# Performance work log

Measured on AMD Instinct MI355X. Metric: run time of the kernel, lower is better.

The kernel has to match this reference:

```python
import jax, jax.numpy as jnp
import numpy as np

B, T, C, H = 128, 200, 171, 1024  # batch, timesteps, frame_dim, hidden


def setup_inputs() -> dict:
    key = jax.random.key(0)
    ks = jax.random.split(key, 16)
    s = 1.0 / np.sqrt(H)  # PyTorch default init range for LSTMCell/Linear

    def u(k, shape):
        return jax.random.uniform(k, shape, jnp.float32, -s, s)

    inp = {
        "seq": jax.random.normal(ks[0], (B, T, C), jnp.float32),
        # LSTMCell 1: input C -> hidden H
        "W_ih1": u(ks[1], (4 * H, C)), "W_hh1": u(ks[2], (4 * H, H)),
        "b_ih1": u(ks[3], (4 * H,)),   "b_hh1": u(ks[4], (4 * H,)),
        # LSTMCell 2: H -> H
        "W_ih2": u(ks[5], (4 * H, H)), "W_hh2": u(ks[6], (4 * H, H)),
        "b_ih2": u(ks[7], (4 * H,)),   "b_hh2": u(ks[8], (4 * H,)),
        # LSTMCell 3: H -> H
        "W_ih3": u(ks[9], (4 * H, H)), "W_hh3": u(ks[10], (4 * H, H)),
        "b_ih3": u(ks[11], (4 * H,)),  "b_hh3": u(ks[12], (4 * H,)),
        # decoder Linear: H -> C
        "W_dec": u(ks[13], (C, H)), "b_dec": u(ks[14], (C,)),
        "cond": 5, "gt": 5,
    }
    return inp


def _lstm_cell(x, h, c, W_ih, W_hh, b_ih, b_hh):
    # PyTorch LSTMCell gate order: i, f, g, o
    gates = x @ W_ih.T + b_ih + h @ W_hh.T + b_hh
    i, f, g, o = jnp.split(gates, 4, axis=-1)
    c_new = jax.nn.sigmoid(f) * c + jax.nn.sigmoid(i) * jnp.tanh(g)
    h_new = jax.nn.sigmoid(o) * jnp.tanh(c_new)
    return h_new, c_new


def reference(seq, W_ih1, W_hh1, b_ih1, b_hh1,
              W_ih2, W_hh2, b_ih2, b_hh2,
              W_ih3, W_hh3, b_ih3, b_hh3,
              W_dec, b_dec, cond, gt):
    Bb, Tt, Cc = seq.shape
    Hh = W_hh1.shape[1]
    # Static teacher-forcing pattern: gt ground-truth steps, then cond self-conditioned steps.
    pattern = jnp.asarray(np.array(([True] * gt + [False] * cond) * 100, dtype=bool)[:Tt])

    def step(carry, xs):
        h1, c1, h2, c2, h3, c3, xo = carry
        x_t, use_gt = xs
        x = jnp.where(use_gt, x_t, xo)
        h1, c1 = _lstm_cell(x, h1, c1, W_ih1, W_hh1, b_ih1, b_hh1)
        h2, c2 = _lstm_cell(h1, h2, c2, W_ih2, W_hh2, b_ih2, b_hh2)
        h3, c3 = _lstm_cell(h2, h3, c3, W_ih3, W_hh3, b_ih3, b_hh3)
        xo = h3 @ W_dec.T + b_dec
        return (h1, c1, h2, c2, h3, c3, xo), xo

    z = jnp.zeros((Bb, Hh), seq.dtype)
    init = (z, z, z, z, z, z, jnp.zeros((Bb, Cc), seq.dtype))
    _, out = jax.lax.scan(step, init, (seq.transpose(1, 0, 2), pattern))
    return out.transpose(1, 0, 2)  # [B, T, C]
```

## Files before the change

### kernel.cpp

```cpp
#include <hip/hip_runtime.h>

#define TT 200
#define BB 128
#define CC 171
#define HH 1024

typedef __attribute__((ext_vector_type(8))) short short8;
typedef __attribute__((ext_vector_type(4))) float f32x4;

__device__ __forceinline__ unsigned short f2bf(float f) {
  unsigned int u = __float_as_uint(f);
  u += 0x7fff + ((u >> 16) & 1);
  return (unsigned short)(u >> 16);
}
__device__ __forceinline__ float sigmoidf_(float x) { return 1.f / (1.f + __expf(-x)); }

__device__ __forceinline__ int4 ld_coh16(const void* p) {
  int4 r;
  asm volatile("global_load_dwordx4 %0, %1, off sc0 sc1" : "=v"(r) : "v"(p));
  return r;
}
__device__ __forceinline__ void st_coh2(void* p, unsigned int v) {
  asm volatile("global_store_short %0, %1, off sc0 sc1" :: "v"(p), "v"(v) : "memory");
}
__device__ __forceinline__ void drain_vm() {
  asm volatile("s_waitcnt vmcnt(0)" ::: "memory");
}

__device__ __forceinline__ void gridbar(int* bar, int wg, int tid, int epoch) {
  drain_vm();
  __syncthreads();
  if (tid == 0) {
    int g = wg & 7;
    int o = __hip_atomic_fetch_add(&bar[g * 32], 1, __ATOMIC_RELAXED, __HIP_MEMORY_SCOPE_AGENT);
    if (o == epoch * 32 - 1) {
      int m = __hip_atomic_fetch_add(&bar[960], 1, __ATOMIC_RELAXED, __HIP_MEMORY_SCOPE_AGENT);
      if (m == epoch * 8 - 1) {
#pragma unroll
        for (int i = 0; i < 8; ++i)
          __hip_atomic_store(&bar[(16 + i) * 32], epoch, __ATOMIC_RELAXED, __HIP_MEMORY_SCOPE_AGENT);
      }
    }
    while (__hip_atomic_load(&bar[(16 + g) * 32], __ATOMIC_RELAXED, __HIP_MEMORY_SCOPE_AGENT) < epoch)
      __builtin_amdgcn_s_sleep(1);
  }
  asm volatile("" ::: "memory");
  __syncthreads();
}

template<int NKT1, int NKTTOT, bool A1SEQ>
__device__ __forceinline__ void lstm_phase(
    const void* A1v, int sA1,
    const unsigned short* __restrict__ A2, int sA2,
    const unsigned short* __restrict__ Wa, int sWa,
    const unsigned short* __restrict__ Wb, int sWb,
    const float* __restrict__ bias,
    float& creg, unsigned short* __restrict__ Hout,
    char* smem, int m0, int n0, int ntile, int tid)
{
  constexpr int BASE = NKTTOT / 4;
  constexpr int REM = NKTTOT % 4;
  constexpr int MAXKT = BASE + (REM ? 1 : 0);

  const int wave = tid >> 6, lane = tid & 63;
  const int grp = wave >> 2, gw = wave & 3;
  const int lrow = lane >> 3, lj = lane & 7;
  const int fl = lane & 15, fh = lane >> 4;

  const int kt0 = grp * BASE + min(grp, REM);
  const int ktn = BASE + (grp < REM ? 1 : 0);

  char* Ar = smem + grp * 32768;
  const int row = gw * 8 + lrow;
  int4 areg[MAXKT];
#pragma unroll
  for (int i = 0; i < MAXKT; ++i) {
    if (i < ktn) {
      int kt = kt0 + i;
      if (kt < NKT1) {
        if constexpr (A1SEQ) {
          const float* srow = (const float*)A1v + (size_t)(m0 + row) * sA1;
          int c0 = kt * 64 + ((lj ^ (row & 7)) << 3);
          unsigned int w[4];
#pragma unroll
          for (int j = 0; j < 4; ++j) {
            int ca = c0 + 2 * j, cb = c0 + 2 * j + 1;
            float va = (ca < CC) ? srow[ca] : 0.f;
            float vb = (cb < CC) ? srow[cb] : 0.f;
            w[j] = (unsigned int)f2bf(va) | ((unsigned int)f2bf(vb) << 16);
          }
          areg[i] = make_int4(w[0], w[1], w[2], w[3]);
        } else {
          const unsigned short* srow = (const unsigned short*)A1v + (size_t)(m0 + row) * sA1;
          areg[i] = ld_coh16(srow + kt * 64 + ((lj ^ (row & 7)) << 3));
        }
      } else {
        areg[i] = ld_coh16(A2 + (size_t)(m0 + row) * sA2 + (kt - NKT1) * 64 + ((lj ^ (row & 7)) << 3));
      }
    }
  }
  drain_vm();
#pragma unroll
  for (int i = 0; i < MAXKT; ++i)
    if (i < ktn) *(int4*)(Ar + i * 4096 + row * 128 + lj * 16) = areg[i];
  __syncthreads();

  f32x4 acc0 = {0.f, 0.f, 0.f, 0.f}, acc1 = {0.f, 0.f, 0.f, 0.f};
  const int wrowi = n0 + gw * 16 + fl;
  const int swz = (fl & 7) << 4;
#pragma unroll
  for (int i = 0; i < MAXKT; ++i) {
    if (i < ktn) {
      int kt = kt0 + i;
      const unsigned short* wr = (kt < NKT1)
          ? Wa + (size_t)wrowi * sWa + kt * 64 + fh * 8
          : Wb + (size_t)wrowi * sWb + (kt - NKT1) * 64 + fh * 8;
#pragma unroll
      for (int kk = 0; kk < 2; ++kk) {
        short8 b0 = *(const short8*)(wr + kk * 32);
        int colb = kk * 64 + fh * 16;
        short8 a0 = *(const short8*)(Ar + i * 4096 + fl * 128 + (colb ^ swz));
        short8 a1 = *(const short8*)(Ar + i * 4096 + (16 + fl) * 128 + (colb ^ swz));
        acc0 = __builtin_amdgcn_mfma_f32_16x16x32_bf16(a0, b0, acc0, 0, 0, 0);
        acc1 = __builtin_amdgcn_mfma_f32_16x16x32_bf16(a1, b0, acc1, 0, 0, 0);
      }
    }
  }

  __syncthreads();
  float* ex = (float*)smem;
#pragma unroll
  for (int r = 0; r < 4; ++r) {
    ex[((grp * 4 + gw) * 32 + fh * 4 + r) * 16 + fl] = acc0[r];
    ex[((grp * 4 + gw) * 32 + 16 + fh * 4 + r) * 16 + fl] = acc1[r];
  }
  __syncthreads();
  if (tid < 512) {
    int urow = tid >> 4, uu = tid & 15;
    float g4[4];
#pragma unroll
    for (int gg = 0; gg < 4; ++gg) {
      float s = ex[(gg * 32 + urow) * 16 + uu] + ex[((4 + gg) * 32 + urow) * 16 + uu]
              + ex[((8 + gg) * 32 + urow) * 16 + uu] + ex[((12 + gg) * 32 + urow) * 16 + uu];
      g4[gg] = s + bias[n0 + gg * 16 + uu];
    }
    float cn = sigmoidf_(g4[1]) * creg + sigmoidf_(g4[0]) * tanhf(g4[2]);
    creg = cn;
    st_coh2(Hout + (size_t)(m0 + urow) * HH + ntile * 16 + uu,
            (unsigned int)f2bf(sigmoidf_(g4[3]) * tanhf(cn)));
  }
}

__device__ __forceinline__ void dec_out(
    const unsigned short* __restrict__ H3in, const unsigned short* __restrict__ Wd,
    const float* __restrict__ bd, float* __restrict__ out,
    int t, char* smem, int d, int tid)
{
  const int wave = tid >> 6, lane = tid & 63;
  const int lrow = lane >> 3, lj = lane & 7;
  const int fl = lane & 15, fh = lane >> 4;
  const int ntile = d % 11, mtile = d / 11;
  const int m0 = mtile * 32, n0 = ntile * 16;

  char* Dr = smem + 65536 + wave * 4096;
  int4 r4[4];
#pragma unroll
  for (int j = 0; j < 4; ++j) {
    int row = j * 8 + lrow;
    r4[j] = ld_coh16(H3in + (size_t)(m0 + row) * HH + wave * 64 + ((lj ^ (row & 7)) << 3));
  }
  drain_vm();
#pragma unroll
  for (int j = 0; j < 4; ++j) {
    int row = j * 8 + lrow;
    *(int4*)(Dr + row * 128 + lj * 16) = r4[j];
  }

  f32x4 acc0 = {0.f, 0.f, 0.f, 0.f}, acc1 = {0.f, 0.f, 0.f, 0.f};
  const unsigned short* Wrow = Wd + (size_t)(n0 + fl) * HH + wave * 64 + fh * 8;
  const int swz = (fl & 7) << 4;
#pragma unroll
  for (int kk = 0; kk < 2; ++kk) {
    short8 b0 = *(const short8*)(Wrow + kk * 32);
    int colb = kk * 64 + fh * 16;
    short8 a0 = *(const short8*)(Dr + fl * 128 + (colb ^ swz));
    short8 a1 = *(const short8*)(Dr + (16 + fl) * 128 + (colb ^ swz));
    acc0 = __builtin_amdgcn_mfma_f32_16x16x32_bf16(a0, b0, acc0, 0, 0, 0);
    acc1 = __builtin_amdgcn_mfma_f32_16x16x32_bf16(a1, b0, acc1, 0, 0, 0);
  }

  float* pex = (float*)(smem + 32768);
#pragma unroll
  for (int r = 0; r < 4; ++r) {
    pex[(wave * 32 + fh * 4 + r) * 16 + fl] = acc0[r];
    pex[(wave * 32 + 16 + fh * 4 + r) * 16 + fl] = acc1[r];
  }
  __syncthreads();
  if (tid < 512) {
    int row = tid >> 4, uu = tid & 15;
    int c = n0 + uu;
    if (c < CC) {
      float s = 0.f;
#pragma unroll
      for (int v = 0; v < 16; ++v) s += pex[(v * 32 + row) * 16 + uu];
      out[(size_t)(m0 + row) * (TT * CC) + (size_t)t * CC + c] = s + bd[c];
    }
  }
}

__global__ __launch_bounds__(1024, 1) void persistent_lstm(
    const unsigned short* __restrict__ Wih1p, const unsigned short* __restrict__ Whh1,
    const unsigned short* __restrict__ Wf, const unsigned short* __restrict__ W2,
    const unsigned short* __restrict__ W3, const unsigned short* __restrict__ Wd,
    const float* __restrict__ B1gt, const float* __restrict__ B1sc,
    const float* __restrict__ B2, const float* __restrict__ B3, const float* __restrict__ Bd,
    unsigned short* __restrict__ Hb, const float* __restrict__ seq, float* __restrict__ out,
    const int* __restrict__ gtp, const int* __restrict__ condp, int* __restrict__ bar)
{
  __shared__ char smem[131072];
  const int wg = blockIdx.x, tid = threadIdx.x;
  const int xg = wg & 7, sl = wg >> 3;
  const int ntile = xg * 8 + (sl >> 2);
  const int m0 = (sl & 3) * 32;
  const int n0 = ntile * 64;
  const int gt = *gtp, cond = *condp;
  const int per = gt + cond;

  int decid = -1;
  if (sl >= 26) { int d = xg * 6 + (sl - 26); if (d < 44) decid = d; }

  unsigned short* H1[2] = { Hb + 0 * BB * HH, Hb + 1 * BB * HH };
  unsigned short* H2[2] = { Hb + 2 * BB * HH, Hb + 3 * BB * HH };
  unsigned short* H3[2] = { Hb + 4 * BB * HH, Hb + 5 * BB * HH };

  float c1 = 0.f, c2 = 0.f, c3 = 0.f;
  int e = 0, tm = 0;
  for (int t = 0; t < TT; ++t) {
    int p = t & 1;
    bool gts = (per > 0) ? (tm < gt) : true;
    if (gts)
      lstm_phase<3, 19, true>(seq + (size_t)t * CC, TT * CC, H1[p], HH,
                              Wih1p, 192, Whh1, HH, B1gt, c1, H1[1 - p], smem, m0, n0, ntile, tid);
    else
      lstm_phase<16, 32, false>(H3[p], HH, H1[p], HH,
                                Wf, HH, Whh1, HH, B1sc, c1, H1[1 - p], smem, m0, n0, ntile, tid);
    if (t > 0 && decid >= 0) dec_out(H3[p], Wd, Bd, out, t - 1, smem, decid, tid);
    gridbar(bar, wg, tid, ++e);
    lstm_phase<16, 32, false>(H1[1 - p], HH, H2[p], HH,
                              W2, 2048, W2 + 1024, 2048, B2, c2, H2[1 - p], smem, m0, n0, ntile, tid);
    gridbar(bar, wg, tid, ++e);
    lstm_phase<16, 32, false>(H2[1 - p], HH, H3[p], HH,
                              W3, 2048, W3 + 1024, 2048, B3, c3, H3[1 - p], smem, m0, n0, ntile, tid);
    gridbar(bar, wg, tid, ++e);
    if (++tm == per) tm = 0;
  }
  if (decid >= 0) dec_out(H3[0], Wd, Bd, out, TT - 1, smem, decid, tid);
}

__device__ __forceinline__ int perm_orig_row(int np) {
  return ((np >> 4) & 3) * HH + ((np >> 6) << 4) + (np & 15);
}

__global__ void conv_wih1p(const float* __restrict__ Wih, unsigned short* __restrict__ dst) {
  int np = blockIdx.x, k = threadIdx.x;
  int n = perm_orig_row(np);
  dst[(size_t)np * 192 + k] = f2bf((k < CC) ? Wih[(size_t)n * CC + k] : 0.f);
}

__global__ void conv_whh1(const float* __restrict__ Whh, unsigned short* __restrict__ dst) {
  int np = blockIdx.y, k = blockIdx.x * 256 + threadIdx.x;
  int n = perm_orig_row(np);
  dst[(size_t)np * HH + k] = f2bf(Whh[(size_t)n * HH + k]);
}

__global__ void conv_w23(const float* __restrict__ Wih, const float* __restrict__ Whh,
                         unsigned short* __restrict__ dst) {
  int k = blockIdx.x * 256 + threadIdx.x;
  int np = blockIdx.y;
  int n = perm_orig_row(np);
  float v = (k < HH) ? Wih[(size_t)n * HH + k] : Whh[(size_t)n * HH + (k - HH)];
  dst[(size_t)np * 2048 + k] = f2bf(v);
}

__global__ void conv_wd(const float* __restrict__ Wsrc, unsigned short* __restrict__ dst) {
  int k = blockIdx.x * 256 + threadIdx.x;
  int row = blockIdx.y;
  dst[(size_t)row * HH + k] = f2bf((row < CC) ? Wsrc[(size_t)row * HH + k] : 0.f);
}

__global__ void wf_gemm(const float* __restrict__ Wih1, const float* __restrict__ Wdec,
                        unsigned short* __restrict__ Wfo) {
  int j = blockIdx.x * 256 + threadIdx.x;
  int np = blockIdx.y;
  int n = perm_orig_row(np);
  const float* wr = Wih1 + (size_t)n * CC;
  float acc = 0.f;
  for (int c = 0; c < CC; ++c) acc = fmaf(wr[c], Wdec[(size_t)c * HH + j], acc);
  Wfo[(size_t)np * HH + j] = f2bf(acc);
}

__global__ void bias_all(const float* bi1, const float* bh1, const float* Wih1, const float* bdec,
                         const float* bi2, const float* bh2, const float* bi3, const float* bh3,
                         float* o1gt, float* o1sc, float* o2, float* o3, float* od) {
  int idx = blockIdx.x * 256 + threadIdx.x;
  if (idx < 4096) {
    int n = perm_orig_row(idx);
    float b = bi1[n] + bh1[n];
    o1gt[idx] = b;
    const float* wr = Wih1 + (size_t)n * CC;
    float acc = 0.f;
    for (int c = 0; c < CC; ++c) acc = fmaf(wr[c], bdec[c], acc);
    o1sc[idx] = b + acc;
  } else if (idx < 8192) {
    int np = idx - 4096; int n = perm_orig_row(np);
    o2[np] = bi2[n] + bh2[n];
  } else if (idx < 12288) {
    int np = idx - 8192; int n = perm_orig_row(np);
    o3[np] = bi3[n] + bh3[n];
  } else if (idx < 12464) {
    int c2 = idx - 12288;
    od[c2] = (c2 < CC) ? bdec[c2] : 0.f;
  }
}

__global__ void init_state(unsigned short* __restrict__ Hall, int* __restrict__ bar) {
  int idx = blockIdx.x * blockDim.x + threadIdx.x;
  if (idx < 6 * BB * HH) Hall[idx] = 0;
  if (idx < 1024) bar[idx] = 0;
}

extern "C" void kernel_launch(void* const* d_in, const int* in_sizes, int n_in,
                              void* d_out, int out_size, void* d_ws, size_t ws_size,
                              hipStream_t stream)
{
  const float* seq   = (const float*)d_in[0];
  const float* W_ih1 = (const float*)d_in[1];
  const float* W_hh1 = (const float*)d_in[2];
  const float* b_ih1 = (const float*)d_in[3];
  const float* b_hh1 = (const float*)d_in[4];
  const float* W_ih2 = (const float*)d_in[5];
  const float* W_hh2 = (const float*)d_in[6];
  const float* b_ih2 = (const float*)d_in[7];
  const float* b_hh2 = (const float*)d_in[8];
  const float* W_ih3 = (const float*)d_in[9];
  const float* W_hh3 = (const float*)d_in[10];
  const float* b_ih3 = (const float*)d_in[11];
  const float* b_hh3 = (const float*)d_in[12];
  const float* W_dec = (const float*)d_in[13];
  const float* b_dec = (const float*)d_in[14];
  const int* condp   = (const int*)d_in[15];
  const int* gtp     = (const int*)d_in[16];
  float* out = (float*)d_out;
  char* ws = (char*)d_ws;

  if (ws_size < 53908480) return;

  unsigned short* Wih1p = (unsigned short*)(ws + 0);
  unsigned short* Whh1  = (unsigned short*)(ws + 1572864);
  unsigned short* Wf    = (unsigned short*)(ws + 9961472);
  unsigned short* W2    = (unsigned short*)(ws + 18350080);
  unsigned short* W3    = (unsigned short*)(ws + 35127296);
  unsigned short* Wd    = (unsigned short*)(ws + 51904512);
  float* B1gt = (float*)(ws + 52264960);
  float* B1sc = (float*)(ws + 52281344);
  float* B2   = (float*)(ws + 52297728);
  float* B3   = (float*)(ws + 52314112);
  float* Bd   = (float*)(ws + 52330496);
  unsigned short* Hbase = (unsigned short*)(ws + 52331520);
  int* bar = (int*)(ws + 53904384);

  conv_wih1p<<<dim3(4096),    192, 0, stream>>>(W_ih1, Wih1p);
  conv_whh1 <<<dim3(4, 4096), 256, 0, stream>>>(W_hh1, Whh1);
  wf_gemm   <<<dim3(4, 4096), 256, 0, stream>>>(W_ih1, W_dec, Wf);
  conv_w23  <<<dim3(8, 4096), 256, 0, stream>>>(W_ih2, W_hh2, W2);
  conv_w23  <<<dim3(8, 4096), 256, 0, stream>>>(W_ih3, W_hh3, W3);
  conv_wd   <<<dim3(4, 176),  256, 0, stream>>>(W_dec, Wd);
  bias_all  <<<dim3(49),      256, 0, stream>>>(b_ih1, b_hh1, W_ih1, b_dec,
                                                b_ih2, b_hh2, b_ih3, b_hh3,
                                                B1gt, B1sc, B2, B3, Bd);
  init_state<<<dim3(3072),    256, 0, stream>>>(Hbase, bar);

  persistent_lstm<<<dim3(256), dim3(1024), 0, stream>>>(
      Wih1p, Whh1, Wf, W2, W3, Wd, B1gt, B1sc, B2, B3, Bd,
      Hbase, seq, out, gtp, condp, bar);
}
```

Measured before the change: 8.043 ms.

## Replace grid barrier with per-batch-group barriers and prefetch recurrent operands

Replaces the full-grid two-level barrier with per-batch-group barriers of 64 workgroups, since each 32-row batch slice depends only on its own rows. The recurrent-state operands (previous h of the same layer) are prefetched before the barrier and consumed first, while the fresh input operand is loaded after it. The decoder work is reassigned so each batch group computes its own rows. Raw s_barrier with explicit lgkmcnt waits replaces __syncthreads. This adds subtle memory-ordering risk: the group barrier no longer drains all stores first, and launch bounds change.

```diff
diff --git a/kernel.cpp b/kernel.cpp
--- a/kernel.cpp
+++ b/kernel.cpp
@@ -26,142 +26,214 @@
 __device__ __forceinline__ void drain_vm() {
   asm volatile("s_waitcnt vmcnt(0)" ::: "memory");
 }
-
-__device__ __forceinline__ void gridbar(int* bar, int wg, int tid, int epoch) {
+__device__ __forceinline__ void wait4() {
+  asm volatile("s_waitcnt vmcnt(4)" ::: "memory");
+}
+__device__ __forceinline__ void bar_lds() {
+  asm volatile("s_waitcnt lgkmcnt(0)" ::: "memory");
+  __builtin_amdgcn_s_barrier();
+  asm volatile("" ::: "memory");
+}
+
+__device__ __forceinline__ void groupbar(int* B, int tid, int epoch) {
+  __builtin_amdgcn_s_barrier();
+  if (tid == 0) {
+    if (__hip_atomic_fetch_add(&B[0], 1, __ATOMIC_RELAXED, __HIP_MEMORY_SCOPE_AGENT) == epoch * 64 - 1)
+      __hip_atomic_store(&B[32], epoch, __ATOMIC_RELAXED, __HIP_MEMORY_SCOPE_AGENT);
+    while (__hip_atomic_load(&B[32], __ATOMIC_RELAXED, __HIP_MEMORY_SCOPE_AGENT) < epoch)
+      __builtin_amdgcn_s_sleep(1);
+  }
+  asm volatile("" ::: "memory");
+  __builtin_amdgcn_s_barrier();
+  asm volatile("" ::: "memory");
+}
+
+struct Pre4 { int4 v[4]; };
+struct Pre5 { int4 v[5]; };
+
+__device__ __forceinline__ void prefetch_old(const unsigned short* A2, int sA2,
+    int m0, int grp, int row, int lj, Pre4& P) {
+  const unsigned short* base = A2 + (size_t)(m0 + row) * sA2 + ((lj ^ (row & 7)) << 3);
+#pragma unroll
+  for (int j = 0; j < 4; ++j)
+    P.v[j] = ld_coh16(base + (grp * 4 + j) * 64);
+}
+
+__device__ __forceinline__ void prefetch_gtl1(const float* seqt,
+    const unsigned short* H1old, int m0, int grp, int row, int lj, Pre5& P) {
+  const int kt0 = grp * 5;
+  const int ktn = 4 + (grp < 3 ? 1 : 0);
+  const float* srow = seqt + (size_t)(m0 + row) * (TT * CC);
+  const unsigned short* hbase = H1old + (size_t)(m0 + row) * HH + ((lj ^ (row & 7)) << 3);
+#pragma unroll
+  for (int i = 0; i < 5; ++i) {
+    if (i < ktn) {
+      int kt = kt0 + i;
+      if (kt < 3) {
+        int c0 = kt * 64 + ((lj ^ (row & 7)) << 3);
+        unsigned int w[4];
+#pragma unroll
+        for (int jj = 0; jj < 4; ++jj) {
+          int ca = c0 + 2 * jj, cb = c0 + 2 * jj + 1;
+          float va = (ca < CC) ? srow[ca] : 0.f;
+          float vb = (cb < CC) ? srow[cb] : 0.f;
+          w[jj] = (unsigned int)f2bf(va) | ((unsigned int)f2bf(vb) << 16);
+        }
+        P.v[i] = make_int4(w[0], w[1], w[2], w[3]);
+      } else {
+        P.v[i] = ld_coh16(hbase + (kt - 3) * 64);
+      }
+    }
+  }
   drain_vm();
-  __syncthreads();
-  if (tid == 0) {
-    int g = wg & 7;
-    int o = __hip_atomic_fetch_add(&bar[g * 32], 1, __ATOMIC_RELAXED, __HIP_MEMORY_SCOPE_AGENT);
-    if (o == epoch * 32 - 1) {
-      int m = __hip_atomic_fetch_add(&bar[960], 1, __ATOMIC_RELAXED, __HIP_MEMORY_SCOPE_AGENT);
-      if (m == epoch * 8 - 1) {
-#pragma unroll
-        for (int i = 0; i < 8; ++i)
-          __hip_atomic_store(&bar[(16 + i) * 32], epoch, __ATOMIC_RELAXED, __HIP_MEMORY_SCOPE_AGENT);
-      }
-    }
-    while (__hip_atomic_load(&bar[(16 + g) * 32], __ATOMIC_RELAXED, __HIP_MEMORY_SCOPE_AGENT) < epoch)
-      __builtin_amdgcn_s_sleep(1);
-  }
-  asm volatile("" ::: "memory");
-  __syncthreads();
-}
-
-template<int NKT1, int NKTTOT, bool A1SEQ>
-__device__ __forceinline__ void lstm_phase(
-    const void* A1v, int sA1,
-    const unsigned short* __restrict__ A2, int sA2,
+}
+
+__device__ __forceinline__ void exchange_cell(f32x4 acc0, f32x4 acc1,
+    const float* bias, float& creg, unsigned short* Hout,
+    char* smem, int m0, int n0, int ntile, int tid) {
+  const int wave = tid >> 6, lane = tid & 63;
+  const int grp = wave >> 2, gw = wave & 3;
+  const int fl = lane & 15, fh = lane >> 4;
+  bar_lds();
+  float* ex = (float*)smem;
+#pragma unroll
+  for (int r = 0; r < 4; ++r) {
+    ex[((grp * 4 + gw) * 32 + fh * 4 + r) * 16 + fl] = acc0[r];
+    ex[((grp * 4 + gw) * 32 + 16 + fh * 4 + r) * 16 + fl] = acc1[r];
+  }
+  bar_lds();
+  if (tid < 512) {
+    int urow = tid >> 4, uu = tid & 15;
+    float g4[4];
+#pragma unroll
+    for (int gg = 0; gg < 4; ++gg) {
+      float s = ex[(gg * 32 + urow) * 16 + uu] + ex[((4 + gg) * 32 + urow) * 16 + uu]
+              + ex[((8 + gg) * 32 + urow) * 16 + uu] + ex[((12 + gg) * 32 + urow) * 16 + uu];
+      g4[gg] = s + bias[n0 + gg * 16 + uu];
+    }
+    float cn = sigmoidf_(g4[1]) * creg + sigmoidf_(g4[0]) * tanhf(g4[2]);
+    creg = cn;
+    st_coh2(Hout + (size_t)(m0 + urow) * HH + ntile * 16 + uu,
+            (unsigned int)f2bf(sigmoidf_(g4[3]) * tanhf(cn)));
+  }
+}
+
+__device__ __forceinline__ void lstm_split(
+    const unsigned short* __restrict__ A1, int sA1,
     const unsigned short* __restrict__ Wa, int sWa,
     const unsigned short* __restrict__ Wb, int sWb,
     const float* __restrict__ bias,
     float& creg, unsigned short* __restrict__ Hout,
-    char* smem, int m0, int n0, int ntile, int tid)
+    char* smem, int m0, int n0, int ntile, int tid, const Pre4& P)
 {
-  constexpr int BASE = NKTTOT / 4;
-  constexpr int REM = NKTTOT % 4;
-  constexpr int MAXKT = BASE + (REM ? 1 : 0);
-
   const int wave = tid >> 6, lane = tid & 63;
   const int grp = wave >> 2, gw = wave & 3;
   const int lrow = lane >> 3, lj = lane & 7;
   const int fl = lane & 15, fh = lane >> 4;
-
-  const int kt0 = grp * BASE + min(grp, REM);
-  const int ktn = BASE + (grp < REM ? 1 : 0);
-
-  char* Ar = smem + grp * 32768;
   const int row = gw * 8 + lrow;
-  int4 areg[MAXKT];
-#pragma unroll
-  for (int i = 0; i < MAXKT; ++i) {
+  const int swz = (fl & 7) << 4;
+  const int wrowi = n0 + gw * 16 + fl;
+  char* G = smem + grp * 32768;
+
+  int4 anew[4];
+  const unsigned short* nbase = A1 + (size_t)(m0 + row) * sA1 + ((lj ^ (row & 7)) << 3);
+#pragma unroll
+  for (int j = 0; j < 4; ++j)
+    anew[j] = ld_coh16(nbase + (grp * 4 + j) * 64);
+  wait4();
+#pragma unroll
+  for (int j = 0; j < 4; ++j)
+    *(int4*)(G + (4 + j) * 4096 + row * 128 + lj * 16) = P.v[j];
+  bar_lds();
+
+  f32x4 acc0 = {0.f, 0.f, 0.f, 0.f}, acc1 = {0.f, 0.f, 0.f, 0.f};
+  const unsigned short* wbr = Wb + (size_t)wrowi * sWb + fh * 8;
+#pragma unroll
+  for (int j = 0; j < 4; ++j) {
+#pragma unroll
+    for (int kk = 0; kk < 2; ++kk) {
+      short8 b0 = *(const short8*)(wbr + (grp * 4 + j) * 64 + kk * 32);
+      int colb = kk * 64 + fh * 16;
+      short8 a0 = *(const short8*)(G + (4 + j) * 4096 + fl * 128 + (colb ^ swz));
+      short8 a1 = *(const short8*)(G + (4 + j) * 4096 + (16 + fl) * 128 + (colb ^ swz));
+      acc0 = __builtin_amdgcn_mfma_f32_16x16x32_bf16(a0, b0, acc0, 0, 0, 0);
+      acc1 = __builtin_amdgcn_mfma_f32_16x16x32_bf16(a1, b0, acc1, 0, 0, 0);
+    }
+  }
+  drain_vm();
+#pragma unroll
+  for (int j = 0; j < 4; ++j)
+    *(int4*)(G + j * 4096 + row * 128 + lj * 16) = anew[j];
+  bar_lds();
+  const unsigned short* war = Wa + (size_t)wrowi * sWa + fh * 8;
+#pragma unroll
+  for (int j = 0; j < 4; ++j) {
+#pragma unroll
+    for (int kk = 0; kk < 2; ++kk) {
+      short8 b0 = *(const short8*)(war + (grp * 4 + j) * 64 + kk * 32);
+      int colb = kk * 64 + fh * 16;
+      short8 a0 = *(const short8*)(G + j * 4096 + fl * 128 + (colb ^ swz));
+      short8 a1 = *(const short8*)(G + j * 4096 + (16 + fl) * 128 + (colb ^ swz));
+      acc0 = __builtin_amdgcn_mfma_f32_16x16x32_bf16(a0, b0, acc0, 0, 0, 0);
+      acc1 = __builtin_amdgcn_mfma_f32_16x16x32_bf16(a1, b0, acc1, 0, 0, 0);
+    }
+  }
+  exchange_cell(acc0, acc1, bias, creg, Hout, smem, m0, n0, ntile, tid);
+}
+
+__device__ __forceinline__ void lstm_gtl1(const Pre5& P,
+    const unsigned short* __restrict__ Wih1p, const unsigned short* __restrict__ Whh1,
+    const float* __restrict__ bias,
+    float& creg, unsigned short* __restrict__ Hout,
+    char* smem, int m0, int n0, int ntile, int tid)
+{
+  const int wave = tid >> 6, lane = tid & 63;
+  const int grp = wave >> 2, gw = wave & 3;
+  const int lrow = lane >> 3, lj = lane & 7;
+  const int fl = lane & 15, fh = lane >> 4;
+  const int row = gw * 8 + lrow;
+  const int swz = (fl & 7) << 4;
+  const int wrowi = n0 + gw * 16 + fl;
+  const int kt0 = grp * 5;
+  const int ktn = 4 + (grp < 3 ? 1 : 0);
+  char* G = smem + grp * 32768;
+
+#pragma unroll
+  for (int i = 0; i < 5; ++i)
+    if (i < ktn) *(int4*)(G + i * 4096 + row * 128 + lj * 16) = P.v[i];
+  bar_lds();
+
+  f32x4 acc0 = {0.f, 0.f, 0.f, 0.f}, acc1 = {0.f, 0.f, 0.f, 0.f};
+#pragma unroll
+  for (int i = 0; i < 5; ++i) {
     if (i < ktn) {
       int kt = kt0 + i;
-      if (kt < NKT1) {
-        if constexpr (A1SEQ) {
-          const float* srow = (const float*)A1v + (size_t)(m0 + row) * sA1;
-          int c0 = kt * 64 + ((lj ^ (row & 7)) << 3);
-          unsigned int w[4];
-#pragma unroll
-          for (int j = 0; j < 4; ++j) {
-            int ca = c0 + 2 * j, cb = c0 + 2 * j + 1;
-            float va = (ca < CC) ? srow[ca] : 0.f;
-            float vb = (cb < CC) ? srow[cb] : 0.f;
-            w[j] = (unsigned int)f2bf(va) | ((unsigned int)f2bf(vb) << 16);
-          }
-          areg[i] = make_int4(w[0], w[1], w[2], w[3]);
-        } else {
-          const unsigned short* srow = (const unsigned short*)A1v + (size_t)(m0 + row) * sA1;
-          areg[i] = ld_coh16(srow + kt * 64 + ((lj ^ (row & 7)) << 3));
-        }
-      } else {
-        areg[i] = ld_coh16(A2 + (size_t)(m0 + row) * sA2 + (kt - NKT1) * 64 + ((lj ^ (row & 7)) << 3));
-      }
-    }
-  }
-  drain_vm();
-#pragma unroll
-  for (int i = 0; i < MAXKT; ++i)
-    if (i < ktn) *(int4*)(Ar + i * 4096 + row * 128 + lj * 16) = areg[i];
-  __syncthreads();
-
-  f32x4 acc0 = {0.f, 0.f, 0.f, 0.f}, acc1 = {0.f, 0.f, 0.f, 0.f};
-  const int wrowi = n0 + gw * 16 + fl;
-  const int swz = (fl & 7) << 4;
-#pragma unroll
-  for (int i = 0; i < MAXKT; ++i) {
-    if (i < ktn) {
-      int kt = kt0 + i;
-      const unsigned short* wr = (kt < NKT1)
-          ? Wa + (size_t)wrowi * sWa + kt * 64 + fh * 8
-          : Wb + (size_t)wrowi * sWb + (kt - NKT1) * 64 + fh * 8;
+      const unsigned short* wr = (kt < 3)
+          ? Wih1p + (size_t)wrowi * 192 + kt * 64 + fh * 8
+          : Whh1 + (size_t)wrowi * HH + (kt - 3) * 64 + fh * 8;
 #pragma unroll
       for (int kk = 0; kk < 2; ++kk) {
         short8 b0 = *(const short8*)(wr + kk * 32);
         int colb = kk * 64 + fh * 16;
-        short8 a0 = *(const short8*)(Ar + i * 4096 + fl * 128 + (colb ^ swz));
-        short8 a1 = *(const short8*)(Ar + i * 4096 + (16 + fl) * 128 + (colb ^ swz));
+        short8 a0 = *(const short8*)(G + i * 4096 + fl * 128 + (colb ^ swz));
+        short8 a1 = *(const short8*)(G + i * 4096 + (16 + fl) * 128 + (colb ^ swz));
         acc0 = __builtin_amdgcn_mfma_f32_16x16x32_bf16(a0, b0, acc0, 0, 0, 0);
         acc1 = __builtin_amdgcn_mfma_f32_16x16x32_bf16(a1, b0, acc1, 0, 0, 0);
       }
     }
   }
-
-  __syncthreads();
-  float* ex = (float*)smem;
-#pragma unroll
-  for (int r = 0; r < 4; ++r) {
-    ex[((grp * 4 + gw) * 32 + fh * 4 + r) * 16 + fl] = acc0[r];
-    ex[((grp * 4 + gw) * 32 + 16 + fh * 4 + r) * 16 + fl] = acc1[r];
-  }
-  __syncthreads();
-  if (tid < 512) {
-    int urow = tid >> 4, uu = tid & 15;
-    float g4[4];
-#pragma unroll
-    for (int gg = 0; gg < 4; ++gg) {
-      float s = ex[(gg * 32 + urow) * 16 + uu] + ex[((4 + gg) * 32 + urow) * 16 + uu]
-              + ex[((8 + gg) * 32 + urow) * 16 + uu] + ex[((12 + gg) * 32 + urow) * 16 + uu];
-      g4[gg] = s + bias[n0 + gg * 16 + uu];
-    }
-    float cn = sigmoidf_(g4[1]) * creg + sigmoidf_(g4[0]) * tanhf(g4[2]);
-    creg = cn;
-    st_coh2(Hout + (size_t)(m0 + urow) * HH + ntile * 16 + uu,
-            (unsigned int)f2bf(sigmoidf_(g4[3]) * tanhf(cn)));
-  }
+  exchange_cell(acc0, acc1, bias, creg, Hout, smem, m0, n0, ntile, tid);
 }
 
 __device__ __forceinline__ void dec_out(
     const unsigned short* __restrict__ H3in, const unsigned short* __restrict__ Wd,
     const float* __restrict__ bd, float* __restrict__ out,
-    int t, char* smem, int d, int tid)
+    int t, char* smem, int d, int tid, int m0)
 {
   const int wave = tid >> 6, lane = tid & 63;
   const int lrow = lane >> 3, lj = lane & 7;
   const int fl = lane & 15, fh = lane >> 4;
-  const int ntile = d % 11, mtile = d / 11;
-  const int m0 = mtile * 32, n0 = ntile * 16;
-
+  const int n0 = d * 16;
   char* Dr = smem + 65536 + wave * 4096;
   int4 r4[4];
 #pragma unroll
@@ -175,7 +247,6 @@
     int row = j * 8 + lrow;
     *(int4*)(Dr + row * 128 + lj * 16) = r4[j];
   }
-
   f32x4 acc0 = {0.f, 0.f, 0.f, 0.f}, acc1 = {0.f, 0.f, 0.f, 0.f};
   const unsigned short* Wrow = Wd + (size_t)(n0 + fl) * HH + wave * 64 + fh * 8;
   const int swz = (fl & 7) << 4;
@@ -188,27 +259,26 @@
     acc0 = __builtin_amdgcn_mfma_f32_16x16x32_bf16(a0, b0, acc0, 0, 0, 0);
     acc1 = __builtin_amdgcn_mfma_f32_16x16x32_bf16(a1, b0, acc1, 0, 0, 0);
   }
-
   float* pex = (float*)(smem + 32768);
 #pragma unroll
   for (int r = 0; r < 4; ++r) {
     pex[(wave * 32 + fh * 4 + r) * 16 + fl] = acc0[r];
     pex[(wave * 32 + 16 + fh * 4 + r) * 16 + fl] = acc1[r];
   }
-  __syncthreads();
+  bar_lds();
   if (tid < 512) {
-    int row = tid >> 4, uu = tid & 15;
+    int rrow = tid >> 4, uu = tid & 15;
     int c = n0 + uu;
     if (c < CC) {
       float s = 0.f;
 #pragma unroll
-      for (int v = 0; v < 16; ++v) s += pex[(v * 32 + row) * 16 + uu];
-      out[(size_t)(m0 + row) * (TT * CC) + (size_t)t * CC + c] = s + bd[c];
-    }
-  }
-}
-
-__global__ __launch_bounds__(1024, 1) void persistent_lstm(
+      for (int v = 0; v < 16; ++v) s += pex[(v * 32 + rrow) * 16 + uu];
+      out[(size_t)(m0 + rrow) * (TT * CC) + (size_t)t * CC + c] = s + bd[c];
+    }
+  }
+}
+
+__global__ __launch_bounds__(1024, 4) void persistent_lstm(
     const unsigned short* __restrict__ Wih1p, const unsigned short* __restrict__ Whh1,
     const unsigned short* __restrict__ Wf, const unsigned short* __restrict__ W2,
     const unsigned short* __restrict__ W3, const unsigned short* __restrict__ Wd,
@@ -221,40 +291,57 @@
   const int wg = blockIdx.x, tid = threadIdx.x;
   const int xg = wg & 7, sl = wg >> 3;
   const int ntile = xg * 8 + (sl >> 2);
-  const int m0 = (sl & 3) * 32;
+  const int mgrp = sl & 3;
+  const int m0 = mgrp * 32;
   const int n0 = ntile * 64;
   const int gt = *gtp, cond = *condp;
   const int per = gt + cond;
-
-  int decid = -1;
-  if (sl >= 26) { int d = xg * 6 + (sl - 26); if (d < 44) decid = d; }
+  const int lane = tid & 63, wave = tid >> 6;
+  const int grp = wave >> 2, gw = wave & 3;
+  const int lrow = lane >> 3, lj = lane & 7;
+  const int row = gw * 8 + lrow;
+
+  int dd = ((ntile & 7) << 3) | (ntile >> 3);
+  const int decid = (dd < 11) ? dd : -1;
 
   unsigned short* H1[2] = { Hb + 0 * BB * HH, Hb + 1 * BB * HH };
   unsigned short* H2[2] = { Hb + 2 * BB * HH, Hb + 3 * BB * HH };
   unsigned short* H3[2] = { Hb + 4 * BB * HH, Hb + 5 * BB * HH };
+  int* B = bar + mgrp * 256;
 
   float c1 = 0.f, c2 = 0.f, c3 = 0.f;
+  Pre4 aold; Pre5 a1pre;
   int e = 0, tm = 0;
+  bool gts = (per > 0) ? (0 < gt) : true;
+  if (gts) prefetch_gtl1(seq, H1[0], m0, grp, row, lj, a1pre);
+  else     prefetch_old(H1[0], HH, m0, grp, row, lj, aold);
+
   for (int t = 0; t < TT; ++t) {
     int p = t & 1;
-    bool gts = (per > 0) ? (tm < gt) : true;
-    if (gts)
-      lstm_phase<3, 19, true>(seq + (size_t)t * CC, TT * CC, H1[p], HH,
-                              Wih1p, 192, Whh1, HH, B1gt, c1, H1[1 - p], smem, m0, n0, ntile, tid);
-    else
-      lstm_phase<16, 32, false>(H3[p], HH, H1[p], HH,
-                                Wf, HH, Whh1, HH, B1sc, c1, H1[1 - p], smem, m0, n0, ntile, tid);
-    if (t > 0 && decid >= 0) dec_out(H3[p], Wd, Bd, out, t - 1, smem, decid, tid);
-    gridbar(bar, wg, tid, ++e);
-    lstm_phase<16, 32, false>(H1[1 - p], HH, H2[p], HH,
-                              W2, 2048, W2 + 1024, 2048, B2, c2, H2[1 - p], smem, m0, n0, ntile, tid);
-    gridbar(bar, wg, tid, ++e);
-    lstm_phase<16, 32, false>(H2[1 - p], HH, H3[p], HH,
-                              W3, 2048, W3 + 1024, 2048, B3, c3, H3[1 - p], smem, m0, n0, ntile, tid);
-    gridbar(bar, wg, tid, ++e);
-    if (++tm == per) tm = 0;
-  }
-  if (decid >= 0) dec_out(H3[0], Wd, Bd, out, TT - 1, smem, decid, tid);
+    if (gts) lstm_gtl1(a1pre, Wih1p, Whh1, B1gt, c1, H1[1 - p], smem, m0, n0, ntile, tid);
+    else     lstm_split(H3[p], HH, Wf, HH, Whh1, HH, B1sc, c1, H1[1 - p],
+                        smem, m0, n0, ntile, tid, aold);
+    if (decid >= 0 && t > 0) dec_out(H3[p], Wd, Bd, out, t - 1, smem, decid, tid, m0);
+    prefetch_old(H2[p], HH, m0, grp, row, lj, aold);
+    wait4();
+    groupbar(B, tid, ++e);
+    lstm_split(H1[1 - p], HH, W2, 2048, W2 + 1024, 2048, B2, c2, H2[1 - p],
+               smem, m0, n0, ntile, tid, aold);
+    prefetch_old(H3[p], HH, m0, grp, row, lj, aold);
+    wait4();
+    groupbar(B, tid, ++e);
+    lstm_split(H2[1 - p], HH, W3, 2048, W3 + 1024, 2048, B3, c3, H3[1 - p],
+               smem, m0, n0, ntile, tid, aold);
+    int tmn = (tm + 1 == per) ? 0 : tm + 1;
+    bool gtsn = (per > 0) ? (tmn < gt) : true;
+    if (t + 1 < TT) {
+      if (gtsn) prefetch_gtl1(seq + (size_t)(t + 1) * CC, H1[1 - p], m0, grp, row, lj, a1pre);
+      else { prefetch_old(H1[1 - p], HH, m0, grp, row, lj, aold); wait4(); }
+    } else drain_vm();
+    groupbar(B, tid, ++e);
+    tm = tmn; gts = gtsn;
+  }
+  if (decid >= 0) dec_out(H3[0], Wd, Bd, out, TT - 1, smem, decid, tid, m0);
 }
 
 __device__ __forceinline__ int perm_orig_row(int np) {
```

Measured after the change: 7.139 ms. 1.13x faster.
